# Optimization experiments

Measured on AMD Instinct MI355X. Metric: run time of the kernel, lower is better.

The kernel has to match this reference:

```python
import jax, jax.numpy as jnp
import numpy as np

B, S, D, H, F, PD = 2, 2048, 768, 12, 3072, 64


def layer_norm(x, w, b, eps=1e-5):
    m = jnp.mean(x, axis=-1, keepdims=True)
    v = jnp.var(x, axis=-1, keepdims=True)
    return (x - m) / jnp.sqrt(v + eps) * w + b


def setup_inputs() -> dict:
    key = jax.random.key(0)
    ks = jax.random.split(key, 8)
    sc = 0.02
    return {
        "x": jax.random.normal(ks[0], (B, S, D), jnp.float32),
        "ln1_w": jnp.ones((D,), jnp.float32),
        "ln1_b": jnp.zeros((D,), jnp.float32),
        "in_proj_w": jax.random.normal(ks[1], (3 * D, D), jnp.float32) * sc,
        "in_proj_b": jnp.zeros((3 * D,), jnp.float32),
        "phase_w": jax.random.normal(ks[2], (PD, D), jnp.float32) * sc,
        "alpha": jnp.float32(0.5),
        "ff_w1": jax.random.normal(ks[3], (F, D), jnp.float32) * sc,
        "ff_b1": jnp.zeros((F,), jnp.float32),
        "ff_w2": jax.random.normal(ks[4], (D, F), jnp.float32) * sc,
        "ff_b2": jnp.zeros((D,), jnp.float32),
        "ln2_w": jnp.ones((D,), jnp.float32),
        "ln2_b": jnp.zeros((D,), jnp.float32),
    }


def reference(x, ln1_w, ln1_b, in_proj_w, in_proj_b, phase_w, alpha,
              ff_w1, ff_b1, ff_w2, ff_b2, ln2_w, ln2_b):
    Dh = D // H
    xn = layer_norm(x, ln1_w, ln1_b)
    # MultiheadAttention with need_weights=True: only the head-averaged
    # softmax(QK^T/sqrt(Dh)) weights are consumed downstream (attn_out is
    # discarded in the original forward, so V/out_proj are dead code).
    qkv = xn @ in_proj_w.T + in_proj_b                       # [B,S,3D]
    q, k, _ = jnp.split(qkv, 3, axis=-1)
    q = q.reshape(B, S, H, Dh) * (1.0 / np.sqrt(Dh)).astype(np.float32)
    k = k.reshape(B, S, H, Dh)
    scores = jnp.einsum('bqhd,bkhd->bhqk', q, k)             # [B,H,S,S]
    attn_w = jax.nn.softmax(scores, axis=-1).mean(axis=1)    # head-avg [B,S,S]
    phase = jnp.tanh(xn @ phase_w.T)                         # [B,S,64]
    phase_coh = (phase @ phase.swapaxes(-2, -1) + 1.0) * 0.5  # [B,S,S]
    blended = jax.nn.softmax(jnp.log(attn_w + 1e-6) + alpha * phase_coh, axis=-1)
    x = x + blended @ xn                                     # enhanced context
    x2 = layer_norm(x, ln2_w, ln2_b)
    h = jax.nn.gelu(x2 @ ff_w1.T + ff_b1, approximate=False)  # exact GELU (torch default)
    ff = h @ ff_w2.T + ff_b2
    return x + ff
```

## Files before the change

### kernel.cpp

```cpp
#include <hip/hip_runtime.h>
#include <math.h>

typedef unsigned short u16;
typedef short bf8 __attribute__((ext_vector_type(8)));
typedef float f4 __attribute__((ext_vector_type(4)));

#define LOG2E 1.44269504088896340736f

__device__ __forceinline__ u16 f2b(float f) {
  union { float f; unsigned int u; } v; v.f = f;
  unsigned int u = v.u;
  return (u16)((u + 0x7FFFu + ((u >> 16) & 1u)) >> 16);
}
__device__ __forceinline__ float b2f(u16 u) {
  union { unsigned int i; float f; } v; v.i = ((unsigned int)u) << 16; return v.f;
}
__device__ __forceinline__ float ex2(float x) {
#if __has_builtin(__builtin_amdgcn_exp2f)
  return __builtin_amdgcn_exp2f(x);
#else
  return exp2f(x);
#endif
}

template <int N>
__device__ __forceinline__ void waitvm() {
  if constexpr (N == 0)      asm volatile("s_waitcnt vmcnt(0)" ::: "memory");
  else if constexpr (N == 3) asm volatile("s_waitcnt vmcnt(3)" ::: "memory");
  else if constexpr (N == 4) asm volatile("s_waitcnt vmcnt(4)" ::: "memory");
  else if constexpr (N == 6) asm volatile("s_waitcnt vmcnt(6)" ::: "memory");
  else if constexpr (N == 8) asm volatile("s_waitcnt vmcnt(8)" ::: "memory");
}

#define GLOAD_LDS16(gp, lp)                                                          \
  __builtin_amdgcn_global_load_lds(                                                  \
      reinterpret_cast<const __attribute__((address_space(1))) unsigned int*>(       \
          reinterpret_cast<uintptr_t>(gp)),                                          \
      reinterpret_cast<__attribute__((address_space(3))) unsigned int*>(             \
          reinterpret_cast<uintptr_t>(lp)),                                          \
      16, 0, 0)

template <int ISSUES>
__device__ __forceinline__ void stage_sw(const u16* gbase, long ldg, u16* lds,
                                         int wv, int lane) {
#pragma unroll
  for (int is = 0; is < ISSUES; ++is) {
    const int idx = is * 256 + wv * 64 + lane;
    const int r = idx >> 3, cs = idx & 7;
    const u16* gp = gbase + (long)r * ldg + ((cs ^ (r & 7)) << 3);
    GLOAD_LDS16(gp, (char*)lds + is * 4096 + wv * 1024);
  }
}
__device__ __forceinline__ bf8 frag_sw(const u16* lds, int r, int c) {
  return *(const bf8*)((const char*)lds + r * 128 + ((c ^ (r & 7)) << 4));
}

__global__ __launch_bounds__(256) void conv_bf16_k(const float* __restrict__ in,
                                                   u16* __restrict__ out, int n4) {
  int i = blockIdx.x * 256 + threadIdx.x;
  if (i >= n4) return;
  float4 v = ((const float4*)in)[i];
  union { u16 s[4]; uint2 u; } o;
  o.s[0] = f2b(v.x); o.s[1] = f2b(v.y); o.s[2] = f2b(v.z); o.s[3] = f2b(v.w);
  ((uint2*)out)[i] = o.u;
}

__global__ __launch_bounds__(256) void ln_bf16_k(const float* __restrict__ in,
                                                 const float* __restrict__ w,
                                                 const float* __restrict__ b,
                                                 u16* __restrict__ out) {
  const long row = blockIdx.x;
  const float* xr = in + row * 768;
  const int t = threadIdx.x;
  float v[3];
  float s = 0.f, q = 0.f;
#pragma unroll
  for (int i = 0; i < 3; ++i) {
    v[i] = xr[t + 256 * i];
    s += v[i]; q += v[i] * v[i];
  }
#pragma unroll
  for (int off = 1; off < 64; off <<= 1) { s += __shfl_xor(s, off); q += __shfl_xor(q, off); }
  __shared__ float rs[4], rq[4];
  const int wave = t >> 6, lane = t & 63;
  if (lane == 0) { rs[wave] = s; rq[wave] = q; }
  __syncthreads();
  s = rs[0] + rs[1] + rs[2] + rs[3];
  q = rq[0] + rq[1] + rq[2] + rq[3];
  const float mean = s * (1.0f / 768.0f);
  const float var = q * (1.0f / 768.0f) - mean * mean;
  const float rstd = rsqrtf(var + 1e-5f);
  u16* orow = out + row * 768;
#pragma unroll
  for (int i = 0; i < 3; ++i) {
    const int c = t + 256 * i;
    orow[c] = f2b((v[i] - mean) * rstd * w[c] + b[c]);
  }
}

__global__ __launch_bounds__(256) void transp_k(const u16* __restrict__ in,
                                                u16* __restrict__ out) {
  const int d0 = blockIdx.x * 64, s0 = blockIdx.y * 64;
  __shared__ u16 T[64][72];
  const int t = threadIdx.x;
  {
    const int r = t >> 3, c8 = (t & 7) * 8;
#pragma unroll
    for (int p = 0; p < 2; ++p) {
      const int rr = r + 32 * p;
      *(uint4*)&T[rr][c8] = *(const uint4*)&in[(long)(s0 + rr) * 768 + d0 + c8];
    }
  }
  __syncthreads();
  {
    const int d = t >> 3, s8 = (t & 7) * 8;
#pragma unroll
    for (int p = 0; p < 2; ++p) {
      const int dd = d + 32 * p;
      u16 tmp[8];
#pragma unroll
      for (int e = 0; e < 8; ++e) tmp[e] = T[s8 + e][dd];
      *(uint4*)&out[(long)(d0 + dd) * 4096 + s0 + s8] = *(uint4*)tmp;
    }
  }
}

template <int EPI, int TM>
__global__ __launch_bounds__(256) void mgemm3_k(
    const u16* __restrict__ A, int lda, long sA,
    const u16* __restrict__ B, int ldb, long sB,
    const float* __restrict__ bias,
    const float* __restrict__ res, long sR,
    void* __restrict__ O0, long sO, void* __restrict__ O1, void* __restrict__ O2,
    const int M, const int N, const int K) {
  constexpr int WR = (TM == 128) ? 2 : 1;
  constexpr int WC = 4 / WR;
  constexpr int MR = TM / (WR * 16);
  constexpr int NR = 128 / (WC * 16);
  constexpr int AISS = TM / 64;
  constexpr int BISS = 2;
  constexpr int NS = AISS + BISS;
  constexpr int AW = TM * 32;
  constexpr int BW = 128 * 32;
  __shared__ u16 As[2 * AW];
  __shared__ u16 Bs[2 * BW];
  const int t = threadIdx.x;
  const int wv = t >> 6, lane = t & 63;
  const int lr = lane & 15, lg = lane >> 4;
  const int wr = wv / WC, wc = wv % WC;
  const int wrow0 = wr * (MR * 16), wcol0 = wc * (NR * 16);
  const int m0 = blockIdx.y * TM, n0 = blockIdx.x * 128;
  const int bz = blockIdx.z;
  const u16* Ab = A + (long)bz * sA + (long)m0 * lda;
  const u16* Bb = B + (long)bz * sB + (long)n0 * ldb;
  const long zR = (long)bz * sR, zO = (long)bz * sO;

  const u16* ga[AISS];
  const u16* gb[BISS];
#pragma unroll
  for (int is = 0; is < AISS; ++is) {
    const int idx = is * 256 + wv * 64 + lane;
    const int r = idx >> 2, c = idx & 3;
    ga[is] = Ab + (long)r * lda + ((c ^ ((r >> 1) & 3)) << 3);
  }
#pragma unroll
  for (int is = 0; is < BISS; ++is) {
    const int idx = is * 256 + wv * 64 + lane;
    const int r = idx >> 2, c = idx & 3;
    gb[is] = Bb + (long)r * ldb + ((c ^ ((r >> 1) & 3)) << 3);
  }

  int offA[MR], offB[NR];
#pragma unroll
  for (int i = 0; i < MR; ++i) {
    const int r = wrow0 + i * 16 + lr;
    offA[i] = r * 64 + ((lg ^ ((r >> 1) & 3)) << 4);
  }
#pragma unroll
  for (int j = 0; j < NR; ++j) {
    const int r = wcol0 + j * 16 + lr;
    offB[j] = r * 64 + ((lg ^ ((r >> 1) & 3)) << 4);
  }

  f4 acc[MR][NR];
  const f4 fz = {0.f, 0.f, 0.f, 0.f};
#pragma unroll
  for (int i = 0; i < MR; ++i)
#pragma unroll
    for (int j = 0; j < NR; ++j) acc[i][j] = fz;

#pragma unroll
  for (int is = 0; is < AISS; ++is) {
    GLOAD_LDS16(ga[is], (char*)As + is * 4096 + wv * 1024);
    ga[is] += 32;
  }
#pragma unroll
  for (int is = 0; is < BISS; ++is) {
    GLOAD_LDS16(gb[is], (char*)Bs + is * 4096 + wv * 1024);
    gb[is] += 32;
  }

  const int NT = K >> 5;
  int cur = 0;
  for (int kt = 0; kt < NT; ++kt) {
    if (kt + 1 < NT) {
      char* bufA = (char*)(As + (cur ^ 1) * AW);
      char* bufB = (char*)(Bs + (cur ^ 1) * BW);
#pragma unroll
      for (int is = 0; is < AISS; ++is) {
        GLOAD_LDS16(ga[is], bufA + is * 4096 + wv * 1024);
        ga[is] += 32;
      }
#pragma unroll
      for (int is = 0; is < BISS; ++is) {
        GLOAD_LDS16(gb[is], bufB + is * 4096 + wv * 1024);
        gb[is] += 32;
      }
      waitvm<NS>();
    } else {
      waitvm<0>();
    }
    __builtin_amdgcn_s_barrier();
    const char* a = (const char*)(As + cur * AW);
    const char* b = (const char*)(Bs + cur * BW);
    bf8 af[MR], bf[NR];
#pragma unroll
    for (int i = 0; i < MR; ++i) af[i] = *(const bf8*)(a + offA[i]);
#pragma unroll
    for (int j = 0; j < NR; ++j) bf[j] = *(const bf8*)(b + offB[j]);
#pragma unroll
    for (int i = 0; i < MR; ++i)
#pragma unroll
      for (int j = 0; j < NR; ++j)
        acc[i][j] = __builtin_amdgcn_mfma_f32_16x16x32_bf16(af[i], bf[j], acc[i][j], 0, 0, 0);
    __builtin_amdgcn_s_barrier();
    cur ^= 1;
  }

#pragma unroll
  for (int i = 0; i < MR; ++i) {
    const int gr0 = m0 + wrow0 + i * 16 + lg * 4;
#pragma unroll
    for (int j = 0; j < NR; ++j) {
      const int gc = n0 + wcol0 + j * 16 + lr;
#pragma unroll
      for (int r = 0; r < 4; ++r) {
        const long row = gr0 + r;
        float v = acc[i][j][r];
        if (EPI == 0) {
          if (gc < 1536) {
            v += bias[gc];
            if (gc < 768) ((u16*)O0)[row * 768 + gc] = f2b(v * (0.125f * LOG2E));
            else          ((u16*)O1)[row * 768 + gc - 768] = f2b(v);
          } else if (gc < 1600) {
            ((u16*)O2)[row * 64 + gc - 1536] = f2b(tanhf(v));
          }
        } else if (EPI == 3) {
          v += bias[gc];
          ((u16*)O0)[row * N + gc] = f2b(0.5f * v * (1.0f + erff(v * 0.70710678118654752f)));
        } else if (EPI == 4) {
          ((float*)O0)[row * N + gc] = v + bias[gc] + res[row * N + gc];
        } else {
          const float sc = bias[(long)bz * M + row];
          ((float*)O0)[zO + row * N + gc] = v * sc + res[zR + row * N + gc];
        }
      }
    }
  }
}

__global__ __launch_bounds__(256) void attn_stats3(const u16* __restrict__ qb,
                                                   const u16* __restrict__ kb,
                                                   float* __restrict__ Ms_g) {
  const int qt = blockIdx.x, h = blockIdx.y, b = blockIdx.z;
  const int t = threadIdx.x, wv = t >> 6, lane = t & 63;
  const int lr = lane & 15, lg = lane >> 4;
  __shared__ u16 Qs[64 * 64];
  __shared__ u16 Ks[2][128 * 64];
  __shared__ float zbuf[4][64];
  const long q0 = (long)b * 2048 + qt * 64;
  const long kbase = ((long)b * 2048) * 768 + h * 64;
  stage_sw<2>(qb + q0 * 768 + h * 64, 768, Qs, wv, lane);
  stage_sw<4>(kb + kbase, 768, Ks[0], wv, lane);
  waitvm<4>();
  __builtin_amdgcn_s_barrier();

  bf8 aq[4][2];
#pragma unroll
  for (int i = 0; i < 4; ++i)
#pragma unroll
    for (int kk = 0; kk < 2; ++kk)
      aq[i][kk] = frag_sw(Qs, i * 16 + lr, kk * 4 + lg);

  float zp[4][4];
#pragma unroll
  for (int i = 0; i < 4; ++i)
#pragma unroll
    for (int r = 0; r < 4; ++r) zp[i][r] = 0.f;

  const f4 fz = {0.f, 0.f, 0.f, 0.f};
  int cur = 0;
  for (int kt = 0; kt < 16; ++kt) {
    if (kt < 15) {
      stage_sw<4>(kb + kbase + (long)(kt + 1) * 128 * 768, 768, Ks[cur ^ 1], wv, lane);
      waitvm<4>();
    } else {
      waitvm<0>();
    }
    __builtin_amdgcn_s_barrier();
#pragma unroll
    for (int j = 0; j < 2; ++j) {
      const int krow = wv * 32 + j * 16 + lr;
      const bf8 b0 = frag_sw(Ks[cur], krow, lg);
      const bf8 b1 = frag_sw(Ks[cur], krow, 4 + lg);
#pragma unroll
      for (int i = 0; i < 4; ++i) {
        f4 s = fz;
        s = __builtin_amdgcn_mfma_f32_16x16x32_bf16(aq[i][0], b0, s, 0, 0, 0);
        s = __builtin_amdgcn_mfma_f32_16x16x32_bf16(aq[i][1], b1, s, 0, 0, 0);
#pragma unroll
        for (int r = 0; r < 4; ++r) zp[i][r] += ex2(s[r]);
      }
    }
    __builtin_amdgcn_s_barrier();
    cur ^= 1;
  }
#pragma unroll
  for (int i = 0; i < 4; ++i)
#pragma unroll
    for (int r = 0; r < 4; ++r) {
      float z = zp[i][r];
      z += __shfl_xor(z, 1); z += __shfl_xor(z, 2);
      z += __shfl_xor(z, 4); z += __shfl_xor(z, 8);
      zp[i][r] = z;
    }
  if (lr == 0) {
#pragma unroll
    for (int i = 0; i < 4; ++i)
#pragma unroll
      for (int r = 0; r < 4; ++r)
        zbuf[wv][i * 16 + lg * 4 + r] = zp[i][r];
  }
  __syncthreads();
  if (t < 64) {
    const float Z = zbuf[0][t] + zbuf[1][t] + zbuf[2][t] + zbuf[3][t];
    Ms_g[((long)(b * 12 + h)) * 2048 + qt * 64 + t] = log2f(12.0f * Z);
  }
}

__global__ __launch_bounds__(256) void blendpre5(const u16* __restrict__ qb,
                                                 const u16* __restrict__ kb,
                                                 const u16* __restrict__ ph,
                                                 const float* __restrict__ Ms_g,
                                                 const float* __restrict__ alpha_p,
                                                 u16* __restrict__ eb) {
  const int kt = blockIdx.x, qt = blockIdx.y, b = blockIdx.z;
  const int t = threadIdx.x, wv = t >> 6, lane = t & 63;
  const int lr = lane & 15, lg = lane >> 4;
  const int wr = wv >> 1, wc = wv & 1;
  const int q0 = qt * 128, k0 = kt * 128;
  __shared__ u16 Qs[2][128 * 64];
  __shared__ u16 Ks[2][128 * 64];
  __shared__ float Ms[12][128];
  for (int idx = t; idx < 1536; idx += 256)
    Ms[idx >> 7][idx & 127] = Ms_g[((long)(b * 12 + (idx >> 7))) * 2048 + q0 + (idx & 127)];
  asm volatile("s_waitcnt vmcnt(0) lgkmcnt(0)" ::: "memory");
  __builtin_amdgcn_s_barrier();
  const float a2 = alpha_p[0] * 0.5f * LOG2E;

  f4 acc[4][4];
  const f4 fz = {0.f, 0.f, 0.f, 0.f};
#pragma unroll
  for (int i = 0; i < 4; ++i)
#pragma unroll
    for (int j = 0; j < 4; ++j) acc[i][j] = fz;

  const long qrow0 = (long)b * 2048 + q0;
  const long krow0 = (long)b * 2048 + k0;

  stage_sw<4>(qb + qrow0 * 768, 768, Qs[0], wv, lane);
  stage_sw<4>(kb + krow0 * 768, 768, Ks[0], wv, lane);

  int cur = 0;
  for (int h = 0; h < 12; ++h) {
    if (h < 11) {
      stage_sw<4>(qb + qrow0 * 768 + (h + 1) * 64, 768, Qs[cur ^ 1], wv, lane);
      stage_sw<4>(kb + krow0 * 768 + (h + 1) * 64, 768, Ks[cur ^ 1], wv, lane);
      waitvm<8>();
    } else {
      waitvm<0>();
    }
    __builtin_amdgcn_s_barrier();
    bf8 aq0[4], aq1[4], bk0[4], bk1[4];
#pragma unroll
    for (int i = 0; i < 4; ++i) {
      aq0[i] = frag_sw(Qs[cur], wr * 64 + i * 16 + lr, lg);
      aq1[i] = frag_sw(Qs[cur], wr * 64 + i * 16 + lr, 4 + lg);
    }
#pragma unroll
    for (int j = 0; j < 4; ++j) {
      bk0[j] = frag_sw(Ks[cur], wc * 64 + j * 16 + lr, lg);
      bk1[j] = frag_sw(Ks[cur], wc * 64 + j * 16 + lr, 4 + lg);
    }
#pragma unroll
    for (int i = 0; i < 4; ++i) {
      const f4 mv = *(const f4*)&Ms[h][wr * 64 + i * 16 + lg * 4];
      const f4 cin = fz - mv;
#pragma unroll
      for (int j = 0; j < 4; ++j) {
        f4 s = __builtin_amdgcn_mfma_f32_16x16x32_bf16(aq0[i], bk0[j], cin, 0, 0, 0);
        s = __builtin_amdgcn_mfma_f32_16x16x32_bf16(aq1[i], bk1[j], s, 0, 0, 0);
#pragma unroll
        for (int r = 0; r < 4; ++r) acc[i][j][r] += ex2(s[r]);
      }
    }
    __builtin_amdgcn_s_barrier();
    cur ^= 1;
  }

#pragma unroll
  for (int i = 0; i < 4; ++i) {
    const u16* pa = ph + (qrow0 + wr * 64 + i * 16 + lr) * 64;
    const bf8 pa0 = *(const bf8*)(pa + lg * 8);
    const bf8 pa1 = *(const bf8*)(pa + 32 + lg * 8);
#pragma unroll
    for (int j = 0; j < 4; ++j) {
      const u16* pb = ph + (krow0 + wc * 64 + j * 16 + lr) * 64;
      const bf8 pb0 = *(const bf8*)(pb + lg * 8);
      const bf8 pb1 = *(const bf8*)(pb + 32 + lg * 8);
      f4 coh = fz;
      coh = __builtin_amdgcn_mfma_f32_16x16x32_bf16(pa0, pb0, coh, 0, 0, 0);
      coh = __builtin_amdgcn_mfma_f32_16x16x32_bf16(pa1, pb1, coh, 0, 0, 0);
#pragma unroll
      for (int r = 0; r < 4; ++r) {
        const long row = qrow0 + wr * 64 + i * 16 + lg * 4 + r;
        const int col = k0 + wc * 64 + j * 16 + lr;
        const float e = (acc[i][j][r] + 1e-6f) * ex2(a2 * (coh[r] + 1.0f));
        eb[row * 2048 + col] = f2b(e);
      }
    }
  }
}

__global__ __launch_bounds__(256) void rowsum_k(const u16* __restrict__ eb,
                                                float* __restrict__ rinv) {
  const long row = blockIdx.x;
  const int t = threadIdx.x, wv = t >> 6, lane = t & 63;
  const uint4 pv = ((const uint4*)(eb + row * 2048))[t];
  float s = b2f(pv.x & 0xffff) + b2f(pv.x >> 16) + b2f(pv.y & 0xffff) + b2f(pv.y >> 16) +
            b2f(pv.z & 0xffff) + b2f(pv.z >> 16) + b2f(pv.w & 0xffff) + b2f(pv.w >> 16);
#pragma unroll
  for (int off = 1; off < 64; off <<= 1) s += __shfl_xor(s, off);
  __shared__ float red[4];
  if (lane == 0) red[wv] = s;
  __syncthreads();
  if (t == 0) rinv[row] = 1.0f / (red[0] + red[1] + red[2] + red[3]);
}

extern "C" void kernel_launch(void* const* d_in, const int* in_sizes, int n_in,
                              void* d_out, int out_size, void* d_ws, size_t ws_size,
                              hipStream_t stream) {
  (void)in_sizes; (void)n_in; (void)out_size; (void)ws_size;
  const float* x         = (const float*)d_in[0];
  const float* ln1_w     = (const float*)d_in[1];
  const float* ln1_b     = (const float*)d_in[2];
  const float* in_proj_w = (const float*)d_in[3];
  const float* in_proj_b = (const float*)d_in[4];
  const float* phase_w   = (const float*)d_in[5];
  const float* alpha_p   = (const float*)d_in[6];
  const float* ff_w1     = (const float*)d_in[7];
  const float* ff_b1     = (const float*)d_in[8];
  const float* ff_w2     = (const float*)d_in[9];
  const float* ff_b2     = (const float*)d_in[10];
  const float* ln2_w     = (const float*)d_in[11];
  const float* ln2_b     = (const float*)d_in[12];
  float* out = (float*)d_out;

  char* w = (char*)d_ws;
  u16*   xn_b  = (u16*)w;            w += 6291456;
  u16*   xnT_b = (u16*)w;            w += 6291456;
  u16*   ph_b  = (u16*)w;            w += 524288;
  float* Ms_g  = (float*)w;          w += 196608;
  float* xmid  = (float*)w;          w += 12582912;
  char* big = w;
  u16* q_b  = (u16*)big;
  u16* k_b  = (u16*)(big + 6291456);
  u16* eb_b = (u16*)(big + 12582912);
  char* tail = big + 12582912 + 16777216;
  u16* wcat_b = (u16*)tail;
  float* rinv = (float*)(tail + 2555904);
  u16* h_b  = (u16*)big;
  char* wtail = tail + 16777216;
  u16* wff1_b = (u16*)wtail;
  u16* wff2_b = (u16*)(wtail + 4718592);
  u16* x2n_b = xn_b;

  conv_bf16_k<<<(1536 * 768 / 4 + 255) / 256, 256, 0, stream>>>(in_proj_w, wcat_b, 1536 * 768 / 4);
  conv_bf16_k<<<(64 * 768 / 4 + 255) / 256, 256, 0, stream>>>(phase_w, wcat_b + 1536 * 768, 64 * 768 / 4);
  conv_bf16_k<<<(3072 * 768 / 4 + 255) / 256, 256, 0, stream>>>(ff_w1, wff1_b, 3072 * 768 / 4);
  conv_bf16_k<<<(768 * 3072 / 4 + 255) / 256, 256, 0, stream>>>(ff_w2, wff2_b, 768 * 3072 / 4);

  ln_bf16_k<<<4096, 256, 0, stream>>>(x, ln1_w, ln1_b, xn_b);

  mgemm3_k<0, 128><<<dim3(13, 32, 1), 256, 0, stream>>>(
      xn_b, 768, 0, wcat_b, 768, 0, in_proj_b, nullptr, 0,
      q_b, 0, k_b, ph_b, 4096, 1664, 768);

  transp_k<<<dim3(12, 64), 256, 0, stream>>>(xn_b, xnT_b);

  attn_stats3<<<dim3(32, 12, 2), 256, 0, stream>>>(q_b, k_b, Ms_g);

  blendpre5<<<dim3(16, 16, 2), 256, 0, stream>>>(q_b, k_b, ph_b, Ms_g, alpha_p, eb_b);

  rowsum_k<<<4096, 256, 0, stream>>>(eb_b, rinv);

  mgemm3_k<5, 64><<<dim3(6, 32, 2), 256, 0, stream>>>(
      eb_b, 2048, 2048L * 2048, xnT_b, 4096, 2048, rinv, x, 2048L * 768,
      xmid, 2048L * 768, nullptr, nullptr, 2048, 768, 2048);

  ln_bf16_k<<<4096, 256, 0, stream>>>(xmid, ln2_w, ln2_b, x2n_b);

  mgemm3_k<3, 128><<<dim3(24, 32, 1), 256, 0, stream>>>(
      x2n_b, 768, 0, wff1_b, 768, 0, ff_b1, nullptr, 0,
      h_b, 0, nullptr, nullptr, 4096, 3072, 768);

  mgemm3_k<4, 64><<<dim3(6, 64, 1), 256, 0, stream>>>(
      h_b, 3072, 0, wff2_b, 3072, 0, ff_b2, xmid, 0,
      out, 0, nullptr, nullptr, 4096, 768, 3072);
}
```

Measured before the change: 231.2 us.

## Double GEMM K-tile to 64 and remap workgroups across XCDs

The bf16 MFMA GEMM kernel now stages 64-wide K slices per iteration instead of 32. It uses a wider 8-way XOR swizzle and runs two MFMA sub-steps per barrier pair, which halves the number of barrier-synchronised iterations. Block indices are also permuted so consecutive tiles are grouped per XCD, aiming for better L2 reuse. The cost is twice the LDS per block (up to 64KB for TM=128), which can lower occupancy, plus more fragment registers.

```diff
diff --git a/kernel.cpp b/kernel.cpp
--- a/kernel.cpp
+++ b/kernel.cpp
@@ -26,7 +26,6 @@
 template <int N>
 __device__ __forceinline__ void waitvm() {
   if constexpr (N == 0)      asm volatile("s_waitcnt vmcnt(0)" ::: "memory");
-  else if constexpr (N == 3) asm volatile("s_waitcnt vmcnt(3)" ::: "memory");
   else if constexpr (N == 4) asm volatile("s_waitcnt vmcnt(4)" ::: "memory");
   else if constexpr (N == 6) asm volatile("s_waitcnt vmcnt(6)" ::: "memory");
   else if constexpr (N == 8) asm volatile("s_waitcnt vmcnt(8)" ::: "memory");
@@ -126,7 +125,7 @@
 }
 
 template <int EPI, int TM>
-__global__ __launch_bounds__(256) void mgemm3_k(
+__global__ __launch_bounds__(256) void mgemm4_k(
     const u16* __restrict__ A, int lda, long sA,
     const u16* __restrict__ B, int ldb, long sB,
     const float* __restrict__ bias,
@@ -137,11 +136,11 @@
   constexpr int WC = 4 / WR;
   constexpr int MR = TM / (WR * 16);
   constexpr int NR = 128 / (WC * 16);
-  constexpr int AISS = TM / 64;
-  constexpr int BISS = 2;
+  constexpr int AISS = TM / 32;
+  constexpr int BISS = 4;
   constexpr int NS = AISS + BISS;
-  constexpr int AW = TM * 32;
-  constexpr int BW = 128 * 32;
+  constexpr int AW = TM * 64;
+  constexpr int BW = 128 * 64;
   __shared__ u16 As[2 * AW];
   __shared__ u16 Bs[2 * BW];
   const int t = threadIdx.x;
@@ -149,7 +148,14 @@
   const int lr = lane & 15, lg = lane >> 4;
   const int wr = wv / WC, wc = wv % WC;
   const int wrow0 = wr * (MR * 16), wcol0 = wc * (NR * 16);
-  const int m0 = blockIdx.y * TM, n0 = blockIdx.x * 128;
+
+  const int gx = gridDim.x;
+  const int nwg = gx * gridDim.y;
+  const int cpx = nwg >> 3;
+  const int flat = blockIdx.x + gx * blockIdx.y;
+  const int nf = (flat & 7) * cpx + (flat >> 3);
+  const int m0 = (nf / gx) * TM, n0 = (nf % gx) * 128;
+
   const int bz = blockIdx.z;
   const u16* Ab = A + (long)bz * sA + (long)m0 * lda;
   const u16* Bb = B + (long)bz * sB + (long)n0 * ldb;
@@ -160,26 +166,28 @@
 #pragma unroll
   for (int is = 0; is < AISS; ++is) {
     const int idx = is * 256 + wv * 64 + lane;
-    const int r = idx >> 2, c = idx & 3;
-    ga[is] = Ab + (long)r * lda + ((c ^ ((r >> 1) & 3)) << 3);
+    const int r = idx >> 3, cs = idx & 7;
+    ga[is] = Ab + (long)r * lda + ((cs ^ (r & 7)) << 3);
   }
 #pragma unroll
   for (int is = 0; is < BISS; ++is) {
     const int idx = is * 256 + wv * 64 + lane;
-    const int r = idx >> 2, c = idx & 3;
-    gb[is] = Bb + (long)r * ldb + ((c ^ ((r >> 1) & 3)) << 3);
-  }
-
-  int offA[MR], offB[NR];
+    const int r = idx >> 3, cs = idx & 7;
+    gb[is] = Bb + (long)r * ldb + ((cs ^ (r & 7)) << 3);
+  }
+
+  int offA[2][MR], offB[2][NR];
 #pragma unroll
   for (int i = 0; i < MR; ++i) {
     const int r = wrow0 + i * 16 + lr;
-    offA[i] = r * 64 + ((lg ^ ((r >> 1) & 3)) << 4);
+    offA[0][i] = r * 128 + ((lg ^ (r & 7)) << 4);
+    offA[1][i] = r * 128 + (((4 + lg) ^ (r & 7)) << 4);
   }
 #pragma unroll
   for (int j = 0; j < NR; ++j) {
     const int r = wcol0 + j * 16 + lr;
-    offB[j] = r * 64 + ((lg ^ ((r >> 1) & 3)) << 4);
+    offB[0][j] = r * 128 + ((lg ^ (r & 7)) << 4);
+    offB[1][j] = r * 128 + (((4 + lg) ^ (r & 7)) << 4);
   }
 
   f4 acc[MR][NR];
@@ -192,15 +200,15 @@
 #pragma unroll
   for (int is = 0; is < AISS; ++is) {
     GLOAD_LDS16(ga[is], (char*)As + is * 4096 + wv * 1024);
-    ga[is] += 32;
+    ga[is] += 64;
   }
 #pragma unroll
   for (int is = 0; is < BISS; ++is) {
     GLOAD_LDS16(gb[is], (char*)Bs + is * 4096 + wv * 1024);
-    gb[is] += 32;
-  }
-
-  const int NT = K >> 5;
+    gb[is] += 64;
+  }
+
+  const int NT = K >> 6;
   int cur = 0;
   for (int kt = 0; kt < NT; ++kt) {
     if (kt + 1 < NT) {
@@ -209,12 +217,12 @@
 #pragma unroll
       for (int is = 0; is < AISS; ++is) {
         GLOAD_LDS16(ga[is], bufA + is * 4096 + wv * 1024);
-        ga[is] += 32;
+        ga[is] += 64;
       }
 #pragma unroll
       for (int is = 0; is < BISS; ++is) {
         GLOAD_LDS16(gb[is], bufB + is * 4096 + wv * 1024);
-        gb[is] += 32;
+        gb[is] += 64;
       }
       waitvm<NS>();
     } else {
@@ -223,16 +231,21 @@
     __builtin_amdgcn_s_barrier();
     const char* a = (const char*)(As + cur * AW);
     const char* b = (const char*)(Bs + cur * BW);
-    bf8 af[MR], bf[NR];
-#pragma unroll
-    for (int i = 0; i < MR; ++i) af[i] = *(const bf8*)(a + offA[i]);
-#pragma unroll
-    for (int j = 0; j < NR; ++j) bf[j] = *(const bf8*)(b + offB[j]);
-#pragma unroll
-    for (int i = 0; i < MR; ++i)
-#pragma unroll
-      for (int j = 0; j < NR; ++j)
-        acc[i][j] = __builtin_amdgcn_mfma_f32_16x16x32_bf16(af[i], bf[j], acc[i][j], 0, 0, 0);
+    bf8 af[2][MR], bf[2][NR];
+#pragma unroll
+    for (int s = 0; s < 2; ++s) {
+#pragma unroll
+      for (int i = 0; i < MR; ++i) af[s][i] = *(const bf8*)(a + offA[s][i]);
+#pragma unroll
+      for (int j = 0; j < NR; ++j) bf[s][j] = *(const bf8*)(b + offB[s][j]);
+    }
+#pragma unroll
+    for (int s = 0; s < 2; ++s)
+#pragma unroll
+      for (int i = 0; i < MR; ++i)
+#pragma unroll
+        for (int j = 0; j < NR; ++j)
+          acc[i][j] = __builtin_amdgcn_mfma_f32_16x16x32_bf16(af[s][i], bf[s][j], acc[i][j], 0, 0, 0);
     __builtin_amdgcn_s_barrier();
     cur ^= 1;
   }
@@ -502,7 +515,7 @@
 
   ln_bf16_k<<<4096, 256, 0, stream>>>(x, ln1_w, ln1_b, xn_b);
 
-  mgemm3_k<0, 128><<<dim3(13, 32, 1), 256, 0, stream>>>(
+  mgemm4_k<0, 128><<<dim3(13, 32, 1), 256, 0, stream>>>(
       xn_b, 768, 0, wcat_b, 768, 0, in_proj_b, nullptr, 0,
       q_b, 0, k_b, ph_b, 4096, 1664, 768);
 
@@ -514,17 +527,17 @@
 
   rowsum_k<<<4096, 256, 0, stream>>>(eb_b, rinv);
 
-  mgemm3_k<5, 64><<<dim3(6, 32, 2), 256, 0, stream>>>(
+  mgemm4_k<5, 64><<<dim3(6, 32, 2), 256, 0, stream>>>(
       eb_b, 2048, 2048L * 2048, xnT_b, 4096, 2048, rinv, x, 2048L * 768,
       xmid, 2048L * 768, nullptr, nullptr, 2048, 768, 2048);
 
   ln_bf16_k<<<4096, 256, 0, stream>>>(xmid, ln2_w, ln2_b, x2n_b);
 
-  mgemm3_k<3, 128><<<dim3(24, 32, 1), 256, 0, stream>>>(
+  mgemm4_k<3, 128><<<dim3(24, 32, 1), 256, 0, stream>>>(
       x2n_b, 768, 0, wff1_b, 768, 0, ff_b1, nullptr, 0,
       h_b, 0, nullptr, nullptr, 4096, 3072, 768);
 
-  mgemm3_k<4, 64><<<dim3(6, 64, 1), 256, 0, stream>>>(
+  mgemm4_k<4, 64><<<dim3(6, 64, 1), 256, 0, stream>>>(
       h_b, 3072, 0, wff2_b, 3072, 0, ff_b2, xmid, 0,
       out, 0, nullptr, nullptr, 4096, 768, 3072);
 }
```

Result: faster. 213.5 us (-7.7%).
